# Performance work log

Hardware: AMD Instinct MI355X
Metric: run time of the kernel (lower is better)

## Reference

```python
import jax, jax.numpy as jnp
import numpy as np

# scipy.ndimage.gaussian_filter(sigma=1, truncate=4): radius 4, 9-tap kernel on EVERY axis
_R = 4
_xk = np.arange(-_R, _R + 1)
_wk = np.exp(-0.5 * _xk * _xk)
_W1D = (_wk / _wk.sum()).astype(np.float32)


def _sym_idx(n, r):
    # scipy 'reflect' (symmetric, edge repeated) extension indices for any r, any n
    p = np.arange(-r, n + r)
    q = np.mod(p, 2 * n)
    return np.where(q < n, q, 2 * n - 1 - q)


def gauss_filter(x):
    # separable sigma=1 Gaussian over ALL axes (incl. batch & channel), as scipy does
    w = jnp.asarray(_W1D)
    for axis in range(x.ndim):
        n = x.shape[axis]
        idx = jnp.asarray(_sym_idx(n, _R))
        xp = jnp.take(x, idx, axis=axis)  # symmetric-padded along `axis`
        acc = w[0] * jax.lax.slice_in_dim(xp, 0, n, axis=axis)
        for k in range(1, 2 * _R + 1):
            acc = acc + w[k] * jax.lax.slice_in_dim(xp, k, k + n, axis=axis)
        x = acc
    return x


def downsample(x):
    return x[:, :, ::2, ::2, ::2]


def upsample(x):
    # faithful to source: zero-interleave D and H, but zeros are APPENDED along W
    B, C, D, H, W = x.shape
    t = jnp.stack([x, jnp.zeros_like(x)], axis=3).reshape(B, C, 2 * D, H, W)
    t = jnp.stack([t, jnp.zeros_like(t)], axis=4).reshape(B, C, 2 * D, 2 * H, W)
    t = jnp.concatenate([t, jnp.zeros_like(t)], axis=4)  # (B,C,2D,2H,2W), 2nd W-half zero
    return gauss_filter(t * 8.0)


def lap_pyramid(img, max_levels):
    pyr = []
    cur = img
    for _ in range(max_levels):
        filt = gauss_filter(cur)
        down = downsample(filt)
        up = upsample(down)
        pyr.append(cur - up)
        cur = down
    return pyr


def setup_inputs():
    key = jax.random.key(0)
    k1, k2 = jax.random.split(key)
    shape = (2, 1, 64, 256, 256)
    return {
        "input": jax.random.normal(k1, shape, dtype=jnp.float32),
        "target": jax.random.normal(k2, shape, dtype=jnp.float32),
    }


def reference(input, target):
    max_levels = 5
    pyr_in = lap_pyramid(input, max_levels)
    pyr_tg = lap_pyramid(target, max_levels)
    loss = jnp.float32(0.0)
    for a, b in zip(pyr_in, pyr_tg):
        loss = loss + jnp.mean(jnp.abs(a - b))  # F.l1_loss (mean reduction)
    return loss
```

## Files before the change

kernel.cpp:

```cpp
#include <hip/hip_runtime.h>
#include <hip/hip_bf16.h>
#include <math.h>


struct GW { float w[9]; float A, B; };

__device__ __forceinline__ int ridx(int p, int n) {
    int m = 2 * n;
    int q = (p + m) & (m - 1);
    return (q < n) ? q : (m - 1 - q);
}

__device__ __forceinline__ float block_sum256(float v) {
    #pragma unroll
    for (int off = 32; off > 0; off >>= 1) v += __shfl_down(v, off, 64);
    __shared__ float wp[4];
    int tid = threadIdx.x;
    if ((tid & 63) == 0) wp[tid >> 6] = v;
    __syncthreads();
    return wp[0] + wp[1] + wp[2] + wp[3];
}

template<bool WDIFF>
__global__ __launch_bounds__(256)
void k1l0(const float* __restrict__ in, const float* __restrict__ tg,
          float* __restrict__ T1, __hip_bfloat16* __restrict__ DIFF, GW g)
{
    const int H = 256, W = 256, Wd = 128;
    const int x0d = blockIdx.x * 64, y0d = blockIdx.y * 16, slice = blockIdx.z;
    __shared__ float raw[40][136];
    __shared__ float mid[40][64];
    const size_t in_off  = (size_t)slice * H * W;
    const size_t out_off = (size_t)slice * 128 * 128;
    const int tid = threadIdx.x;
    const int gy0 = 2*y0d - 4, gx0 = 2*x0d - 4;
    for (int i = tid; i < 40*32; i += 256) {
        int rr = i >> 5, c4 = (i & 31) + 1;
        int gy = ridx(gy0 + rr, H);
        size_t base = in_off + (size_t)gy * W + gx0 + 4*c4;
        float4 v = *(const float4*)(in + base);
        float4 b = *(const float4*)(tg + base);
        v.x -= b.x; v.y -= b.y; v.z -= b.z; v.w -= b.w;
        *(float4*)&raw[rr][4*c4] = v;
    }
    for (int i = tid; i < 40*8; i += 256) {
        int rr = i >> 3, j = i & 7;
        int cc = (j < 4) ? j : (128 + j);
        int gy = ridx(gy0 + rr, H);
        int gx = ridx(gx0 + cc, W);
        size_t idx = in_off + (size_t)gy * W + gx;
        raw[rr][cc] = in[idx] - tg[idx];
    }
    __syncthreads();
    if (WDIFF) {
        for (int i = tid; i < 32*128; i += 256) {
            int r = i >> 7, c = i & 127;
            DIFF[in_off + (size_t)(2*y0d + r) * W + (2*x0d + c)] =
                __float2bfloat16(raw[4 + r][4 + c]);
        }
    }
    for (int i = tid; i < 40*64; i += 256) {
        int rr = i >> 6, c = i & 63;
        float s = 0.f;
        #pragma unroll
        for (int k = 0; k < 9; ++k) s = fmaf(g.w[k], raw[rr][2*c + k], s);
        mid[rr][c] = s;
    }
    __syncthreads();
    {
        int r = tid >> 6, c = tid & 63;
        int ox = x0d + c;
        #pragma unroll
        for (int j = 0; j < 4; ++j) {
            int oy = y0d + r*4 + j;
            int rb = 2*(r*4 + j);
            float s = 0.f;
            #pragma unroll
            for (int k = 0; k < 9; ++k) s = fmaf(g.w[k], mid[rb + k][c], s);
            T1[out_off + (size_t)oy * Wd + ox] = s;
        }
    }
}

__global__ __launch_bounds__(256)
void k2s(const float* __restrict__ Tin, float* __restrict__ Cout,
         int D, int Dd, int M4, GW g)
{
    long i = (long)blockIdx.x * 256 + threadIdx.x;
    if (i >= (long)Dd * M4) return;
    int zd = (int)(i / M4);
    int q  = (int)(i - (long)zd * M4);
    const float4* T = (const float4*)Tin;
    float4* O = (float4*)Cout;
    float4 s0 = {0,0,0,0}, s1 = {0,0,0,0};
    #pragma unroll
    for (int k = 0; k < 9; ++k) {
        int zp = 2*zd - 4 + k;
        int zk = (zp >= 0 && zp < D) ? zp : ridx(zp, D);
        float4 a = T[(size_t)zk * M4 + q];
        float4 b = T[(size_t)(D + zk) * M4 + q];
        s0.x = fmaf(g.w[k], a.x, s0.x); s0.y = fmaf(g.w[k], a.y, s0.y);
        s0.z = fmaf(g.w[k], a.z, s0.z); s0.w = fmaf(g.w[k], a.w, s0.w);
        s1.x = fmaf(g.w[k], b.x, s1.x); s1.y = fmaf(g.w[k], b.y, s1.y);
        s1.z = fmaf(g.w[k], b.z, s1.z); s1.w = fmaf(g.w[k], b.w, s1.w);
    }
    float4 o0, o1;
    o0.x = g.A*s0.x + g.B*s1.x; o0.y = g.A*s0.y + g.B*s1.y;
    o0.z = g.A*s0.z + g.B*s1.z; o0.w = g.A*s0.w + g.B*s1.w;
    o1.x = g.B*s0.x + g.A*s1.x; o1.y = g.B*s0.y + g.A*s1.y;
    o1.z = g.B*s0.z + g.A*s1.z; o1.w = g.B*s0.w + g.A*s1.w;
    O[(size_t)zd * M4 + q] = o0;
    O[(size_t)(Dd + zd) * M4 + q] = o1;
}

__global__ __launch_bounds__(256)
void k1s(const float* __restrict__ inA, float* __restrict__ out,
         int H, int W, int Hd, int Wd, GW g)
{
    const int x0d = blockIdx.x * 64, y0d = blockIdx.y * 16, slice = blockIdx.z;
    __shared__ float raw[40][136];
    __shared__ float mid[40][64];
    const size_t in_off  = (size_t)slice * H * W;
    const size_t out_off = (size_t)slice * Hd * Wd;
    const int tid = threadIdx.x;
    const int gy0 = 2*y0d - 4, gx0 = 2*x0d - 4;
    if (2*x0d + 127 < W) {
        for (int i = tid; i < 40*32; i += 256) {
            int rr = i >> 5, c4 = (i & 31) + 1;
            int gy = ridx(gy0 + rr, H);
            *(float4*)&raw[rr][4*c4] =
                *(const float4*)(inA + in_off + (size_t)gy * W + gx0 + 4*c4);
        }
        for (int i = tid; i < 40*8; i += 256) {
            int rr = i >> 3, j = i & 7;
            int cc = (j < 4) ? j : (128 + j);
            int gy = ridx(gy0 + rr, H), gx = ridx(gx0 + cc, W);
            raw[rr][cc] = inA[in_off + (size_t)gy * W + gx];
        }
    } else {
        for (int i = tid; i < 40*136; i += 256) {
            int rr = i / 136, cc = i - rr*136;
            int gy = ridx(gy0 + rr, H), gx = ridx(gx0 + cc, W);
            raw[rr][cc] = inA[in_off + (size_t)gy * W + gx];
        }
    }
    __syncthreads();
    for (int i = tid; i < 40*64; i += 256) {
        int rr = i >> 6, c = i & 63;
        float s = 0.f;
        #pragma unroll
        for (int k = 0; k < 9; ++k) s = fmaf(g.w[k], raw[rr][2*c + k], s);
        mid[rr][c] = s;
    }
    __syncthreads();
    {
        int r = tid >> 6, c = tid & 63;
        int ox = x0d + c;
        #pragma unroll
        for (int j = 0; j < 4; ++j) {
            int oy = y0d + r*4 + j;
            if (oy < Hd && ox < Wd) {
                int rb = 2*(r*4 + j);
                float s = 0.f;
                #pragma unroll
                for (int k = 0; k < 9; ++k) s = fmaf(g.w[k], mid[rb + k][c], s);
                out[out_off + (size_t)oy * Wd + ox] = s;
            }
        }
    }
}

struct K4P {
    const float* dn[5];
    const float* cur[5];
    const float* in; const float* tg;
    const __hip_bfloat16* DIFF;
    float* P;
    int use_diff;
    int bo[6];
    GW g;
};

__global__ __launch_bounds__(256)
void k4p(K4P p)
{
    const int Dt[5] = {64,32,16,8,4}, Ht[5] = {256,128,64,32,16};
    __shared__ float vt[20][72];
    __shared__ float mid[20][64];
    const int bid = (int)blockIdx.x;
    int l = 0;
    while (l < 4 && bid >= p.bo[l+1]) ++l;
    const int local = bid - p.bo[l];
    const int D = Dt[l], H = Ht[l], W = H;
    const int Dd = D >> 1, Hd = H >> 1, Wd = W >> 1, Md = Hd * Wd;
    const int ntx = (W + 63) >> 6, nty = (H + 31) >> 5;
    const int s = local / (ntx*nty);
    const int rem = local - s*(ntx*nty);
    const int ty = rem / ntx, tx = rem - ty*ntx;
    const int x0 = tx*64, y0 = ty*32;
    const int b = s / D, z = s - b*D;
    const GW g = p.g;
    const float* dn0 = p.dn[l] + (size_t)b * Dd * Md;
    const float* dn1 = p.dn[l] + (size_t)(1 - b) * Dd * Md;
    const int tid = threadIdx.x;
    const int vy0 = (y0 >> 1) - 2;

    const bool zin = (z >= 4) && (z + 4 < D);
    if (zin && !(z & 1)) {
        const int j0 = (z >> 1) - 2;
        for (int i = tid; i < 20*72; i += 256) {
            int rr = i / 72, cc = i - rr*72;
            int vy = vy0 + rr;
            int txx = x0 - 4 + cc;
            if (txx < 0) txx = -1 - txx;
            float v = 0.f;
            if (vy >= 0 && vy < Hd && txx < Wd) {
                size_t o = (size_t)vy * Wd + txx;
                float s0 = 0.f, s1 = 0.f;
                #pragma unroll
                for (int t = 0; t < 5; ++t) {
                    s0 = fmaf(g.w[2*t], dn0[(size_t)(j0 + t) * Md + o], s0);
                    s1 = fmaf(g.w[2*t], dn1[(size_t)(j0 + t) * Md + o], s1);
                }
                v = 8.f * (g.A*s0 + g.B*s1);
            }
            vt[rr][cc] = v;
        }
    } else if (zin) {
        const int j0 = (z - 3) >> 1;
        for (int i = tid; i < 20*72; i += 256) {
            int rr = i / 72, cc = i - rr*72;
            int vy = vy0 + rr;
            int txx = x0 - 4 + cc;
            if (txx < 0) txx = -1 - txx;
            float v = 0.f;
            if (vy >= 0 && vy < Hd && txx < Wd) {
                size_t o = (size_t)vy * Wd + txx;
                float s0 = 0.f, s1 = 0.f;
                #pragma unroll
                for (int t = 0; t < 4; ++t) {
                    s0 = fmaf(g.w[2*t+1], dn0[(size_t)(j0 + t) * Md + o], s0);
                    s1 = fmaf(g.w[2*t+1], dn1[(size_t)(j0 + t) * Md + o], s1);
                }
                v = 8.f * (g.A*s0 + g.B*s1);
            }
            vt[rr][cc] = v;
        }
    } else {
        for (int i = tid; i < 20*72; i += 256) {
            int rr = i / 72, cc = i - rr*72;
            int vy = vy0 + rr;
            int txx = x0 - 4 + cc;
            if (txx < 0) txx = -1 - txx;
            float v = 0.f;
            if (vy >= 0 && vy < Hd && txx < Wd) {
                size_t o = (size_t)vy * Wd + txx;
                float s0 = 0.f, s1 = 0.f;
                #pragma unroll
                for (int k = 0; k < 9; ++k) {
                    int zk = ridx(z - 4 + k, D);
                    if (!(zk & 1)) {
                        int j = zk >> 1;
                        s0 = fmaf(g.w[k], dn0[(size_t)j * Md + o], s0);
                        s1 = fmaf(g.w[k], dn1[(size_t)j * Md + o], s1);
                    }
                }
                v = 8.f * (g.A*s0 + g.B*s1);
            }
            vt[rr][cc] = v;
        }
    }
    __syncthreads();
    for (int i = tid; i < 20*64; i += 256) {
        int rr = i >> 6, c = i & 63;
        float sv = 0.f;
        #pragma unroll
        for (int k = 0; k < 9; ++k) sv = fmaf(g.w[k], vt[rr][c + k], sv);
        mid[rr][c] = sv;
    }
    __syncthreads();
    const bool yin = (y0 >= 4) && (y0 + 35 < H);
    const int c = tid & 63;
    const int ry_base = (tid >> 6) * 8;
    const int ox = x0 + c;
    const size_t c_off = (size_t)s * H * W;
    const float* curl = (l >= 1) ? p.cur[l] : nullptr;
    float lsum = 0.f;
    #pragma unroll
    for (int j = 0; j < 8; ++j) {
        int ry = ry_base + j;
        int oy = y0 + ry;
        if (ox < W && oy < H) {
            float sv = 0.f;
            if (yin) {
                if (!(j & 1)) {
                    int r0 = ry >> 1;
                    sv = g.w[0]*mid[r0][c] + g.w[2]*mid[r0+1][c] + g.w[4]*mid[r0+2][c]
                       + g.w[6]*mid[r0+3][c] + g.w[8]*mid[r0+4][c];
                } else {
                    int r0 = ((ry - 3) >> 1) + 2;
                    sv = g.w[1]*mid[r0][c] + g.w[3]*mid[r0+1][c]
                       + g.w[5]*mid[r0+2][c] + g.w[7]*mid[r0+3][c];
                }
            } else {
                #pragma unroll
                for (int k = 0; k < 9; ++k) {
                    int gy = ridx(oy - 4 + k, H);
                    if (!(gy & 1)) sv = fmaf(g.w[k], mid[(gy >> 1) - vy0][c], sv);
                }
            }
            size_t idx = c_off + (size_t)oy * W + ox;
            float cv;
            if (l == 0) cv = p.use_diff ? __bfloat162float(p.DIFF[idx])
                                        : (p.in[idx] - p.tg[idx]);
            else        cv = curl[idx];
            lsum += fabsf(cv - sv);
        }
    }
    float tot = block_sum256(lsum);
    if (tid == 0) p.P[bid] = tot / ((float)(2*D) * H * W);
}

__global__ __launch_bounds__(1024)
void kreduce(const float* __restrict__ P, int n, float* __restrict__ out)
{
    float s = 0.f;
    for (int i = threadIdx.x; i < n; i += 1024) s += P[i];
    #pragma unroll
    for (int off = 32; off > 0; off >>= 1) s += __shfl_down(s, off, 64);
    __shared__ float wp[16];
    if ((threadIdx.x & 63) == 0) wp[threadIdx.x >> 6] = s;
    __syncthreads();
    if (threadIdx.x == 0) {
        float t = 0.f;
        #pragma unroll
        for (int w = 0; w < 16; ++w) t += wp[w];
        out[0] = t;
    }
}

extern "C" void kernel_launch(void* const* d_in, const int* in_sizes, int n_in,
                              void* d_out, int out_size, void* d_ws, size_t ws_size,
                              hipStream_t stream)
{
    const float* in = (const float*)d_in[0];
    const float* tg = (const float*)d_in[1];
    float* out = (float*)d_out;

    GW g;
    {
        double u[9], S = 0.0;
        for (int k = 0; k < 9; ++k) { double d = k - 4; u[k] = exp(-0.5 * d * d); S += u[k]; }
        for (int k = 0; k < 9; ++k) g.w[k] = (float)(u[k] / S);
        g.A = (float)((2.0*u[0] + u[1] + u[3] + u[4]) / S);
        g.B = (float)((u[1] + 2.0*u[2] + u[3]) / S);
    }

    float* T1  = (float*)d_ws;
    float* C1  = T1  + 2097152;
    float* C2  = C1  + 1048576;
    float* C3  = C2  + 131072;
    float* C4  = C3  + 16384;
    float* C5  = C4  + 2048;
    float* Tl1 = C5  + 256;
    float* Tl2 = Tl1 + 262144;
    float* Tl3 = Tl2 + 32768;
    float* Tl4 = Tl3 + 4096;
    float* P   = Tl4 + 512;
    float* wend = P + 8192;
    __hip_bfloat16* DIFF = (__hip_bfloat16*)wend;
    const size_t base_bytes = (size_t)((char*)wend - (char*)d_ws);
    const size_t diff_bytes = (size_t)2 * 64 * 256 * 256 * sizeof(__hip_bfloat16);
    const int use_diff = (ws_size >= base_bytes + diff_bytes) ? 1 : 0;

    dim3 blk(256);

    if (use_diff) k1l0<true ><<<dim3(2,8,128), blk, 0, stream>>>(in, tg, T1, DIFF, g);
    else          k1l0<false><<<dim3(2,8,128), blk, 0, stream>>>(in, tg, T1, nullptr, g);

    k2s<<<dim3(512), blk, 0, stream>>>(T1, C1, 64, 32, 4096, g);

    k1s<<<dim3(1,4,64), blk, 0, stream>>>(C1, Tl1, 128, 128, 64, 64, g);
    k2s<<<dim3(64),     blk, 0, stream>>>(Tl1, C2, 32, 16, 1024, g);
    k1s<<<dim3(1,2,32), blk, 0, stream>>>(C2, Tl2, 64, 64, 32, 32, g);
    k2s<<<dim3(8),      blk, 0, stream>>>(Tl2, C3, 16, 8, 256, g);
    k1s<<<dim3(1,1,16), blk, 0, stream>>>(C3, Tl3, 32, 32, 16, 16, g);
    k2s<<<dim3(1),      blk, 0, stream>>>(Tl3, C4, 8, 4, 64, g);
    k1s<<<dim3(1,1,8),  blk, 0, stream>>>(C4, Tl4, 16, 16, 8, 8, g);
    k2s<<<dim3(1),      blk, 0, stream>>>(Tl4, C5, 4, 2, 16, g);

    K4P prm;
    prm.dn[0] = C1; prm.dn[1] = C2; prm.dn[2] = C3; prm.dn[3] = C4; prm.dn[4] = C5;
    prm.cur[0] = nullptr; prm.cur[1] = C1; prm.cur[2] = C2; prm.cur[3] = C3; prm.cur[4] = C4;
    prm.in = in; prm.tg = tg;
    prm.DIFF = use_diff ? DIFF : nullptr;
    prm.P = P; prm.use_diff = use_diff;
    prm.g = g;
    prm.bo[0] = 0; prm.bo[1] = 4096; prm.bo[2] = 4608;
    prm.bo[3] = 4672; prm.bo[4] = 4688; prm.bo[5] = 4696;
    k4p<<<dim3(4696), blk, 0, stream>>>(prm);

    kreduce<<<1, 1024, 0, stream>>>(P, 4696, out);
}
```

Baseline: 119.2 us.

## Pair z-slices per block, share depth loads, and exploit zero W-half in level 0

The level-0 loss blocks now cover only the x range affected by the upsampled signal, which is nonzero in just the first W-half plus the filter halo. For the rest of that half, where the upsample is zero, k1l0 sums |in-tg| directly into the partials. The bf16 DIFF write is shrunk to match. k4pz handles two adjacent z slices per block, so the even and odd depth taps come from one set of float4 loads of the downsampled volume, and the vt/mid tiles are doubled. This cuts grid size and global reads, at the cost of more shared memory and register pressure per block.

```diff
diff --git a/kernel.cpp b/kernel.cpp
--- a/kernel.cpp
+++ b/kernel.cpp
@@ -24,7 +24,8 @@
 template<bool WDIFF>
 __global__ __launch_bounds__(256)
 void k1l0(const float* __restrict__ in, const float* __restrict__ tg,
-          float* __restrict__ T1, __hip_bfloat16* __restrict__ DIFF, GW g)
+          float* __restrict__ T1, __hip_bfloat16* __restrict__ DIFF,
+          float* __restrict__ P, GW g)
 {
     const int H = 256, W = 256, Wd = 128;
     const int x0d = blockIdx.x * 64, y0d = blockIdx.y * 16, slice = blockIdx.z;
@@ -53,11 +54,29 @@
     }
     __syncthreads();
     if (WDIFF) {
-        for (int i = tid; i < 32*128; i += 256) {
-            int r = i >> 7, c = i & 127;
-            DIFF[in_off + (size_t)(2*y0d + r) * W + (2*x0d + c)] =
-                __float2bfloat16(raw[4 + r][4 + c]);
-        }
+        if (blockIdx.x == 0) {
+            for (int i = tid; i < 32*128; i += 256) {
+                int r = i >> 7, c = i & 127;
+                DIFF[in_off + (size_t)(2*y0d + r) * W + c] =
+                    __float2bfloat16(raw[4 + r][4 + c]);
+            }
+        } else {
+            for (int i = tid; i < 32*4; i += 256) {
+                int r = i >> 2, c = i & 3;
+                DIFF[in_off + (size_t)(2*y0d + r) * W + 128 + c] =
+                    __float2bfloat16(raw[4 + r][4 + c]);
+            }
+        }
+    }
+    if (blockIdx.x == 1) {
+        float lsum = 0.f;
+        for (int i = tid; i < 32*124; i += 256) {
+            int r = i / 124, c = i - r*124;
+            lsum += fabsf(raw[4 + r][8 + c]);
+        }
+        float tot = block_sum256(lsum);
+        if (tid == 0)
+            P[blockIdx.y + 8*blockIdx.z] = tot * (1.f / 8388608.f);
     }
     for (int i = tid; i < 40*64; i += 256) {
         int rr = i >> 6, c = i & 63;
@@ -182,143 +201,200 @@
 };
 
 __global__ __launch_bounds__(256)
-void k4p(K4P p)
+void k4pz(K4P p)
 {
     const int Dt[5] = {64,32,16,8,4}, Ht[5] = {256,128,64,32,16};
-    __shared__ float vt[20][72];
-    __shared__ float mid[20][64];
+    __shared__ float vt[2][20][72];
+    __shared__ float mid[2][20][64];
     const int bid = (int)blockIdx.x;
     int l = 0;
     while (l < 4 && bid >= p.bo[l+1]) ++l;
     const int local = bid - p.bo[l];
     const int D = Dt[l], H = Ht[l], W = H;
     const int Dd = D >> 1, Hd = H >> 1, Wd = W >> 1, Md = Hd * Wd;
-    const int ntx = (W + 63) >> 6, nty = (H + 31) >> 5;
-    const int s = local / (ntx*nty);
-    const int rem = local - s*(ntx*nty);
-    const int ty = rem / ntx, tx = rem - ty*ntx;
-    const int x0 = tx*64, y0 = ty*32;
-    const int b = s / D, z = s - b*D;
+    const int ntx = (l == 0) ? 3 : ((W + 63) >> 6);
+    const int nty = (H + 31) >> 5;
+    const int ntiles = ntx * nty;
+    const int pairidx = local / ntiles;
+    const int rem = local - pairidx * ntiles;
+    const int ty = rem / ntx, tx = rem - ty * ntx;
+    const int x0 = tx * 64, y0 = ty * 32;
+    const int b = pairidx / Dd, m = pairidx - b * Dd;
+    const int z0 = 2 * m;
     const GW g = p.g;
     const float* dn0 = p.dn[l] + (size_t)b * Dd * Md;
     const float* dn1 = p.dn[l] + (size_t)(1 - b) * Dd * Md;
     const int tid = threadIdx.x;
     const int vy0 = (y0 >> 1) - 2;
 
-    const bool zin = (z >= 4) && (z + 4 < D);
-    if (zin && !(z & 1)) {
-        const int j0 = (z >> 1) - 2;
-        for (int i = tid; i < 20*72; i += 256) {
-            int rr = i / 72, cc = i - rr*72;
+    const bool fastz = (z0 >= 4) && (z0 + 5 < D);
+    if (fastz) {
+        const int j0 = m - 2;
+        for (int i = tid; i < 20*18; i += 256) {
+            int rr = i / 18, gg = i - rr*18;
             int vy = vy0 + rr;
-            int txx = x0 - 4 + cc;
-            if (txx < 0) txx = -1 - txx;
-            float v = 0.f;
-            if (vy >= 0 && vy < Hd && txx < Wd) {
-                size_t o = (size_t)vy * Wd + txx;
-                float s0 = 0.f, s1 = 0.f;
+            bool vyok = (vy >= 0) && (vy < Hd);
+            if (gg == 0) {
                 #pragma unroll
-                for (int t = 0; t < 5; ++t) {
-                    s0 = fmaf(g.w[2*t], dn0[(size_t)(j0 + t) * Md + o], s0);
-                    s1 = fmaf(g.w[2*t], dn1[(size_t)(j0 + t) * Md + o], s1);
+                for (int cc = 0; cc < 4; ++cc) {
+                    int txx = x0 - 4 + cc;
+                    if (txx < 0) txx = -1 - txx;
+                    float e0=0.f, e1=0.f, o0=0.f, o1=0.f;
+                    if (vyok && txx < Wd) {
+                        size_t o = (size_t)vy * Wd + txx;
+                        #pragma unroll
+                        for (int t = 0; t < 5; ++t) {
+                            float a  = dn0[(size_t)(j0+t)*Md + o];
+                            float bb = dn1[(size_t)(j0+t)*Md + o];
+                            float we = g.w[2*t];
+                            e0 = fmaf(we, a, e0); e1 = fmaf(we, bb, e1);
+                            if (t >= 1) {
+                                float wo = g.w[2*t-1];
+                                o0 = fmaf(wo, a, o0); o1 = fmaf(wo, bb, o1);
+                            }
+                        }
+                    }
+                    vt[0][rr][cc] = 8.f*(g.A*e0 + g.B*e1);
+                    vt[1][rr][cc] = 8.f*(g.A*o0 + g.B*o1);
                 }
-                v = 8.f * (g.A*s0 + g.B*s1);
-            }
-            vt[rr][cc] = v;
-        }
-    } else if (zin) {
-        const int j0 = (z - 3) >> 1;
-        for (int i = tid; i < 20*72; i += 256) {
-            int rr = i / 72, cc = i - rr*72;
-            int vy = vy0 + rr;
-            int txx = x0 - 4 + cc;
-            if (txx < 0) txx = -1 - txx;
-            float v = 0.f;
-            if (vy >= 0 && vy < Hd && txx < Wd) {
-                size_t o = (size_t)vy * Wd + txx;
-                float s0 = 0.f, s1 = 0.f;
-                #pragma unroll
-                for (int t = 0; t < 4; ++t) {
-                    s0 = fmaf(g.w[2*t+1], dn0[(size_t)(j0 + t) * Md + o], s0);
-                    s1 = fmaf(g.w[2*t+1], dn1[(size_t)(j0 + t) * Md + o], s1);
+            } else {
+                int cc = 4 * gg;
+                int txx = x0 - 4 + cc;
+                if (vyok && txx + 3 < Wd) {
+                    size_t o = (size_t)vy * Wd + txx;
+                    float4 e0={0,0,0,0}, e1={0,0,0,0}, o0={0,0,0,0}, o1={0,0,0,0};
+                    #pragma unroll
+                    for (int t = 0; t < 5; ++t) {
+                        float4 a  = *(const float4*)(dn0 + (size_t)(j0+t)*Md + o);
+                        float4 bb = *(const float4*)(dn1 + (size_t)(j0+t)*Md + o);
+                        float we = g.w[2*t];
+                        e0.x=fmaf(we,a.x,e0.x); e0.y=fmaf(we,a.y,e0.y);
+                        e0.z=fmaf(we,a.z,e0.z); e0.w=fmaf(we,a.w,e0.w);
+                        e1.x=fmaf(we,bb.x,e1.x); e1.y=fmaf(we,bb.y,e1.y);
+                        e1.z=fmaf(we,bb.z,e1.z); e1.w=fmaf(we,bb.w,e1.w);
+                        if (t >= 1) {
+                            float wo = g.w[2*t-1];
+                            o0.x=fmaf(wo,a.x,o0.x); o0.y=fmaf(wo,a.y,o0.y);
+                            o0.z=fmaf(wo,a.z,o0.z); o0.w=fmaf(wo,a.w,o0.w);
+                            o1.x=fmaf(wo,bb.x,o1.x); o1.y=fmaf(wo,bb.y,o1.y);
+                            o1.z=fmaf(wo,bb.z,o1.z); o1.w=fmaf(wo,bb.w,o1.w);
+                        }
+                    }
+                    vt[0][rr][cc+0] = 8.f*(g.A*e0.x + g.B*e1.x);
+                    vt[0][rr][cc+1] = 8.f*(g.A*e0.y + g.B*e1.y);
+                    vt[0][rr][cc+2] = 8.f*(g.A*e0.z + g.B*e1.z);
+                    vt[0][rr][cc+3] = 8.f*(g.A*e0.w + g.B*e1.w);
+                    vt[1][rr][cc+0] = 8.f*(g.A*o0.x + g.B*o1.x);
+                    vt[1][rr][cc+1] = 8.f*(g.A*o0.y + g.B*o1.y);
+                    vt[1][rr][cc+2] = 8.f*(g.A*o0.z + g.B*o1.z);
+                    vt[1][rr][cc+3] = 8.f*(g.A*o0.w + g.B*o1.w);
+                } else {
+                    #pragma unroll
+                    for (int q4 = 0; q4 < 4; ++q4) {
+                        int txq = txx + q4;
+                        float e0=0.f, e1=0.f, o0=0.f, o1=0.f;
+                        if (vyok && txq < Wd) {
+                            size_t o = (size_t)vy * Wd + txq;
+                            #pragma unroll
+                            for (int t = 0; t < 5; ++t) {
+                                float a  = dn0[(size_t)(j0+t)*Md + o];
+                                float bb = dn1[(size_t)(j0+t)*Md + o];
+                                float we = g.w[2*t];
+                                e0 = fmaf(we, a, e0); e1 = fmaf(we, bb, e1);
+                                if (t >= 1) {
+                                    float wo = g.w[2*t-1];
+                                    o0 = fmaf(wo, a, o0); o1 = fmaf(wo, bb, o1);
+                                }
+                            }
+                        }
+                        vt[0][rr][cc+q4] = 8.f*(g.A*e0 + g.B*e1);
+                        vt[1][rr][cc+q4] = 8.f*(g.A*o0 + g.B*o1);
+                    }
                 }
-                v = 8.f * (g.A*s0 + g.B*s1);
-            }
-            vt[rr][cc] = v;
+            }
         }
     } else {
-        for (int i = tid; i < 20*72; i += 256) {
-            int rr = i / 72, cc = i - rr*72;
-            int vy = vy0 + rr;
-            int txx = x0 - 4 + cc;
-            if (txx < 0) txx = -1 - txx;
-            float v = 0.f;
-            if (vy >= 0 && vy < Hd && txx < Wd) {
-                size_t o = (size_t)vy * Wd + txx;
-                float s0 = 0.f, s1 = 0.f;
-                #pragma unroll
-                for (int k = 0; k < 9; ++k) {
-                    int zk = ridx(z - 4 + k, D);
-                    if (!(zk & 1)) {
-                        int j = zk >> 1;
-                        s0 = fmaf(g.w[k], dn0[(size_t)j * Md + o], s0);
-                        s1 = fmaf(g.w[k], dn1[(size_t)j * Md + o], s1);
-                    }
+        for (int zz = 0; zz < 2; ++zz) {
+            int z = z0 + zz;
+            for (int i = tid; i < 20*72; i += 256) {
+                int rr = i / 72, cc = i - rr*72;
+                int vy = vy0 + rr;
+                int txx = x0 - 4 + cc;
+                if (txx < 0) txx = -1 - txx;
+                float v = 0.f;
+                if (vy >= 0 && vy < Hd && txx < Wd) {
+                    size_t o = (size_t)vy * Wd + txx;
+                    float s0 = 0.f, s1 = 0.f;
+                    #pragma unroll
+                    for (int k = 0; k < 9; ++k) {
+                        int zk = ridx(z - 4 + k, D);
+                        if (!(zk & 1)) {
+                            int j = zk >> 1;
+                            s0 = fmaf(g.w[k], dn0[(size_t)j * Md + o], s0);
+                            s1 = fmaf(g.w[k], dn1[(size_t)j * Md + o], s1);
+                        }
+                    }
+                    v = 8.f * (g.A*s0 + g.B*s1);
                 }
-                v = 8.f * (g.A*s0 + g.B*s1);
-            }
-            vt[rr][cc] = v;
-        }
-    }
-    __syncthreads();
-    for (int i = tid; i < 20*64; i += 256) {
-        int rr = i >> 6, c = i & 63;
+                vt[zz][rr][cc] = v;
+            }
+        }
+    }
+    __syncthreads();
+    for (int i = tid; i < 2*20*64; i += 256) {
+        int zz = i / 1280;
+        int r2 = i - zz*1280;
+        int rr = r2 >> 6, c = r2 & 63;
         float sv = 0.f;
         #pragma unroll
-        for (int k = 0; k < 9; ++k) sv = fmaf(g.w[k], vt[rr][c + k], sv);
-        mid[rr][c] = sv;
+        for (int k = 0; k < 9; ++k) sv = fmaf(g.w[k], vt[zz][rr][c + k], sv);
+        mid[zz][rr][c] = sv;
     }
     __syncthreads();
     const bool yin = (y0 >= 4) && (y0 + 35 < H);
     const int c = tid & 63;
     const int ry_base = (tid >> 6) * 8;
     const int ox = x0 + c;
-    const size_t c_off = (size_t)s * H * W;
+    const int xlim = (l == 0) ? 132 : W;
     const float* curl = (l >= 1) ? p.cur[l] : nullptr;
     float lsum = 0.f;
-    #pragma unroll
-    for (int j = 0; j < 8; ++j) {
-        int ry = ry_base + j;
-        int oy = y0 + ry;
-        if (ox < W && oy < H) {
-            float sv = 0.f;
-            if (yin) {
-                if (!(j & 1)) {
-                    int r0 = ry >> 1;
-                    sv = g.w[0]*mid[r0][c] + g.w[2]*mid[r0+1][c] + g.w[4]*mid[r0+2][c]
-                       + g.w[6]*mid[r0+3][c] + g.w[8]*mid[r0+4][c];
+    for (int zz = 0; zz < 2; ++zz) {
+        const size_t c_off = (size_t)(b*D + z0 + zz) * H * W;
+        #pragma unroll
+        for (int j = 0; j < 8; ++j) {
+            int ry = ry_base + j;
+            int oy = y0 + ry;
+            if (ox < xlim && oy < H) {
+                float sv = 0.f;
+                if (yin) {
+                    if (!(j & 1)) {
+                        int r0 = ry >> 1;
+                        sv = g.w[0]*mid[zz][r0][c] + g.w[2]*mid[zz][r0+1][c]
+                           + g.w[4]*mid[zz][r0+2][c] + g.w[6]*mid[zz][r0+3][c]
+                           + g.w[8]*mid[zz][r0+4][c];
+                    } else {
+                        int r0 = ((ry - 3) >> 1) + 2;
+                        sv = g.w[1]*mid[zz][r0][c] + g.w[3]*mid[zz][r0+1][c]
+                           + g.w[5]*mid[zz][r0+2][c] + g.w[7]*mid[zz][r0+3][c];
+                    }
                 } else {
-                    int r0 = ((ry - 3) >> 1) + 2;
-                    sv = g.w[1]*mid[r0][c] + g.w[3]*mid[r0+1][c]
-                       + g.w[5]*mid[r0+2][c] + g.w[7]*mid[r0+3][c];
+                    #pragma unroll
+                    for (int k = 0; k < 9; ++k) {
+                        int gy = ridx(oy - 4 + k, H);
+                        if (!(gy & 1)) sv = fmaf(g.w[k], mid[zz][(gy >> 1) - vy0][c], sv);
+                    }
                 }
-            } else {
-                #pragma unroll
-                for (int k = 0; k < 9; ++k) {
-                    int gy = ridx(oy - 4 + k, H);
-                    if (!(gy & 1)) sv = fmaf(g.w[k], mid[(gy >> 1) - vy0][c], sv);
-                }
-            }
-            size_t idx = c_off + (size_t)oy * W + ox;
-            float cv;
-            if (l == 0) cv = p.use_diff ? __bfloat162float(p.DIFF[idx])
-                                        : (p.in[idx] - p.tg[idx]);
-            else        cv = curl[idx];
-            lsum += fabsf(cv - sv);
+                size_t idx = c_off + (size_t)oy * W + ox;
+                float cv;
+                if (l == 0) cv = p.use_diff ? __bfloat162float(p.DIFF[idx])
+                                            : (p.in[idx] - p.tg[idx]);
+                else        cv = curl[idx];
+                lsum += fabsf(cv - sv);
+            }
         }
     }
     float tot = block_sum256(lsum);
-    if (tid == 0) p.P[bid] = tot / ((float)(2*D) * H * W);
+    if (tid == 0) p.P[1024 + bid] = tot / ((float)(2*D) * H * W);
 }
 
 __global__ __launch_bounds__(1024)
@@ -367,7 +443,7 @@
     float* Tl3 = Tl2 + 32768;
     float* Tl4 = Tl3 + 4096;
     float* P   = Tl4 + 512;
-    float* wend = P + 8192;
+    float* wend = P + 4096;
     __hip_bfloat16* DIFF = (__hip_bfloat16*)wend;
     const size_t base_bytes = (size_t)((char*)wend - (char*)d_ws);
     const size_t diff_bytes = (size_t)2 * 64 * 256 * 256 * sizeof(__hip_bfloat16);
@@ -375,8 +451,8 @@
 
     dim3 blk(256);
 
-    if (use_diff) k1l0<true ><<<dim3(2,8,128), blk, 0, stream>>>(in, tg, T1, DIFF, g);
-    else          k1l0<false><<<dim3(2,8,128), blk, 0, stream>>>(in, tg, T1, nullptr, g);
+    if (use_diff) k1l0<true ><<<dim3(2,8,128), blk, 0, stream>>>(in, tg, T1, DIFF, P, g);
+    else          k1l0<false><<<dim3(2,8,128), blk, 0, stream>>>(in, tg, T1, nullptr, P, g);
 
     k2s<<<dim3(512), blk, 0, stream>>>(T1, C1, 64, 32, 4096, g);
 
@@ -396,9 +472,9 @@
     prm.DIFF = use_diff ? DIFF : nullptr;
     prm.P = P; prm.use_diff = use_diff;
     prm.g = g;
-    prm.bo[0] = 0; prm.bo[1] = 4096; prm.bo[2] = 4608;
-    prm.bo[3] = 4672; prm.bo[4] = 4688; prm.bo[5] = 4696;
-    k4p<<<dim3(4696), blk, 0, stream>>>(prm);
-
-    kreduce<<<1, 1024, 0, stream>>>(P, 4696, out);
-}
+    prm.bo[0] = 0; prm.bo[1] = 1536; prm.bo[2] = 1792;
+    prm.bo[3] = 1824; prm.bo[4] = 1832; prm.bo[5] = 1836;
+    k4pz<<<dim3(1836), blk, 0, stream>>>(prm);
+
+    kreduce<<<1, 1024, 0, stream>>>(P, 1024 + 1836, out);
+}
```

Result: slower. 122.7 us (+2.9%).

## Exploit zero right-half of upsample to skip level-0 work and precompute depth-upsampled volumes

Applied to the files above, without the earlier changes.

The upsampled level-0 image has a zero right W-half, so beyond column 132 the residual equals the raw difference. That region's L1 sum is now computed directly in the first kernel, and the pyramid loss kernel covers only three x-tiles at level 0. The depth-axis upsample filter for levels 0-2 is precomputed into new V buffers by a fused kernel that runs alongside the next level's downsample. This removes redundant per-tile depth filtering, at the cost of extra workspace and extra global writes and reads for V.

```diff
diff --git a/kernel.cpp b/kernel.cpp
--- a/kernel.cpp
+++ b/kernel.cpp
@@ -24,7 +24,8 @@
 template<bool WDIFF>
 __global__ __launch_bounds__(256)
 void k1l0(const float* __restrict__ in, const float* __restrict__ tg,
-          float* __restrict__ T1, __hip_bfloat16* __restrict__ DIFF, GW g)
+          float* __restrict__ T1, __hip_bfloat16* __restrict__ DIFF,
+          float* __restrict__ P, GW g)
 {
     const int H = 256, W = 256, Wd = 128;
     const int x0d = blockIdx.x * 64, y0d = blockIdx.y * 16, slice = blockIdx.z;
@@ -53,11 +54,29 @@
     }
     __syncthreads();
     if (WDIFF) {
-        for (int i = tid; i < 32*128; i += 256) {
-            int r = i >> 7, c = i & 127;
-            DIFF[in_off + (size_t)(2*y0d + r) * W + (2*x0d + c)] =
-                __float2bfloat16(raw[4 + r][4 + c]);
-        }
+        if (blockIdx.x == 0) {
+            for (int i = tid; i < 32*128; i += 256) {
+                int r = i >> 7, c = i & 127;
+                DIFF[in_off + (size_t)(2*y0d + r) * W + c] =
+                    __float2bfloat16(raw[4 + r][4 + c]);
+            }
+        } else {
+            for (int i = tid; i < 32*4; i += 256) {
+                int r = i >> 2, c = i & 3;
+                DIFF[in_off + (size_t)(2*y0d + r) * W + 128 + c] =
+                    __float2bfloat16(raw[4 + r][4 + c]);
+            }
+        }
+    }
+    if (blockIdx.x == 1) {
+        float lsum = 0.f;
+        for (int i = tid; i < 32*124; i += 256) {
+            int r = i / 124, c = i - r*124;
+            lsum += fabsf(raw[4 + r][8 + c]);
+        }
+        float tot = block_sum256(lsum);
+        if (tid == 0)
+            P[blockIdx.y + 8*blockIdx.z] = tot * (1.f / 8388608.f);
     }
     for (int i = tid; i < 40*64; i += 256) {
         int rr = i >> 6, c = i & 63;
@@ -113,11 +132,10 @@
     O[(size_t)(Dd + zd) * M4 + q] = o1;
 }
 
-__global__ __launch_bounds__(256)
-void k1s(const float* __restrict__ inA, float* __restrict__ out,
-         int H, int W, int Hd, int Wd, GW g)
-{
-    const int x0d = blockIdx.x * 64, y0d = blockIdx.y * 16, slice = blockIdx.z;
+__device__ void dev_k1_slice(const float* __restrict__ inA, float* __restrict__ out,
+                             int x0d, int y0d, int slice, int H, int W, int Hd, int Wd,
+                             const GW& g)
+{
     __shared__ float raw[40][136];
     __shared__ float mid[40][64];
     const size_t in_off  = (size_t)slice * H * W;
@@ -170,8 +188,78 @@
     }
 }
 
+__global__ __launch_bounds__(256)
+void k1s(const float* __restrict__ inA, float* __restrict__ out,
+         int H, int W, int Hd, int Wd, GW g)
+{
+    dev_k1_slice(inA, out, blockIdx.x*64, blockIdx.y*16, blockIdx.z, H, W, Hd, Wd, g);
+}
+
+__device__ void dev_k3_elem(long i, const float4* __restrict__ Dn, float4* __restrict__ O,
+                            int D, int Dd, int M4, const GW& g)
+{
+    if (i >= (long)D * M4) return;
+    int z = (int)(i / M4);
+    int q = (int)(i - (long)z * M4);
+    float4 s0 = {0,0,0,0}, s1 = {0,0,0,0};
+    auto f4 = [](float4& a, float w, const float4 b) {
+        a.x = fmaf(w, b.x, a.x); a.y = fmaf(w, b.y, a.y);
+        a.z = fmaf(w, b.z, a.z); a.w = fmaf(w, b.w, a.w);
+    };
+    if (z >= 4 && z + 4 < D) {
+        if ((z & 1) == 0) {
+            int base = (z >> 1) - 2;
+            #pragma unroll
+            for (int kk = 0; kk < 5; ++kk) {
+                f4(s0, g.w[2*kk], Dn[(size_t)(base + kk) * M4 + q]);
+                f4(s1, g.w[2*kk], Dn[(size_t)(Dd + base + kk) * M4 + q]);
+            }
+        } else {
+            int base = (z - 3) >> 1;
+            #pragma unroll
+            for (int kk = 0; kk < 4; ++kk) {
+                f4(s0, g.w[2*kk+1], Dn[(size_t)(base + kk) * M4 + q]);
+                f4(s1, g.w[2*kk+1], Dn[(size_t)(Dd + base + kk) * M4 + q]);
+            }
+        }
+    } else {
+        #pragma unroll
+        for (int k = 0; k < 9; ++k) {
+            int zk = ridx(z - 4 + k, D);
+            if (!(zk & 1)) {
+                int j = zk >> 1;
+                f4(s0, g.w[k], Dn[(size_t)j * M4 + q]);
+                f4(s1, g.w[k], Dn[(size_t)(Dd + j) * M4 + q]);
+            }
+        }
+    }
+    float4 o0, o1;
+    o0.x = 8.f*(g.A*s0.x + g.B*s1.x); o0.y = 8.f*(g.A*s0.y + g.B*s1.y);
+    o0.z = 8.f*(g.A*s0.z + g.B*s1.z); o0.w = 8.f*(g.A*s0.w + g.B*s1.w);
+    o1.x = 8.f*(g.B*s0.x + g.A*s1.x); o1.y = 8.f*(g.B*s0.y + g.A*s1.y);
+    o1.z = 8.f*(g.B*s0.z + g.A*s1.z); o1.w = 8.f*(g.B*s0.w + g.A*s1.w);
+    O[(size_t)z * M4 + q] = o0;
+    O[(size_t)(D + z) * M4 + q] = o1;
+}
+
+__global__ __launch_bounds__(256)
+void fatk(const float* __restrict__ k1in, float* __restrict__ k1out,
+          int H, int W, int Hd, int Wd, int nty, int n1,
+          const float* __restrict__ dn, float* __restrict__ V,
+          int D, int Dd, int M4, GW g)
+{
+    if ((int)blockIdx.x < n1) {
+        int ty = (int)blockIdx.x % nty, slice = (int)blockIdx.x / nty;
+        dev_k1_slice(k1in, k1out, 0, ty*16, slice, H, W, Hd, Wd, g);
+    } else {
+        long i = (long)((int)blockIdx.x - n1)*256 + threadIdx.x;
+        dev_k3_elem(i, (const float4*)dn, (float4*)V, D, Dd, M4, g);
+    }
+}
+
 struct K4P {
-    const float* dn[5];
+    const float* V[3];
+    const float* dn34[2];
     const float* cur[5];
     const float* in; const float* tg;
     const __hip_bfloat16* DIFF;
@@ -182,7 +270,7 @@
 };
 
 __global__ __launch_bounds__(256)
-void k4p(K4P p)
+void k4all(K4P p)
 {
     const int Dt[5] = {64,32,16,8,4}, Ht[5] = {256,128,64,32,16};
     __shared__ float vt[20][72];
@@ -193,60 +281,33 @@
     const int local = bid - p.bo[l];
     const int D = Dt[l], H = Ht[l], W = H;
     const int Dd = D >> 1, Hd = H >> 1, Wd = W >> 1, Md = Hd * Wd;
-    const int ntx = (W + 63) >> 6, nty = (H + 31) >> 5;
+    const int ntx = (l == 0) ? 3 : ((W + 63) >> 6);
+    const int nty = (H + 31) >> 5;
     const int s = local / (ntx*nty);
     const int rem = local - s*(ntx*nty);
     const int ty = rem / ntx, tx = rem - ty*ntx;
     const int x0 = tx*64, y0 = ty*32;
     const int b = s / D, z = s - b*D;
     const GW g = p.g;
-    const float* dn0 = p.dn[l] + (size_t)b * Dd * Md;
-    const float* dn1 = p.dn[l] + (size_t)(1 - b) * Dd * Md;
     const int tid = threadIdx.x;
     const int vy0 = (y0 >> 1) - 2;
 
-    const bool zin = (z >= 4) && (z + 4 < D);
-    if (zin && !(z & 1)) {
-        const int j0 = (z >> 1) - 2;
+    if (l < 3) {
+        const float* V = p.V[l];
+        const size_t v_off = (size_t)s * Md;
         for (int i = tid; i < 20*72; i += 256) {
             int rr = i / 72, cc = i - rr*72;
             int vy = vy0 + rr;
             int txx = x0 - 4 + cc;
             if (txx < 0) txx = -1 - txx;
             float v = 0.f;
-            if (vy >= 0 && vy < Hd && txx < Wd) {
-                size_t o = (size_t)vy * Wd + txx;
-                float s0 = 0.f, s1 = 0.f;
-                #pragma unroll
-                for (int t = 0; t < 5; ++t) {
-                    s0 = fmaf(g.w[2*t], dn0[(size_t)(j0 + t) * Md + o], s0);
-                    s1 = fmaf(g.w[2*t], dn1[(size_t)(j0 + t) * Md + o], s1);
-                }
-                v = 8.f * (g.A*s0 + g.B*s1);
-            }
+            if (vy >= 0 && vy < Hd && txx < Wd) v = V[v_off + (size_t)vy * Wd + txx];
             vt[rr][cc] = v;
         }
-    } else if (zin) {
-        const int j0 = (z - 3) >> 1;
-        for (int i = tid; i < 20*72; i += 256) {
-            int rr = i / 72, cc = i - rr*72;
-            int vy = vy0 + rr;
-            int txx = x0 - 4 + cc;
-            if (txx < 0) txx = -1 - txx;
-            float v = 0.f;
-            if (vy >= 0 && vy < Hd && txx < Wd) {
-                size_t o = (size_t)vy * Wd + txx;
-                float s0 = 0.f, s1 = 0.f;
-                #pragma unroll
-                for (int t = 0; t < 4; ++t) {
-                    s0 = fmaf(g.w[2*t+1], dn0[(size_t)(j0 + t) * Md + o], s0);
-                    s1 = fmaf(g.w[2*t+1], dn1[(size_t)(j0 + t) * Md + o], s1);
-                }
-                v = 8.f * (g.A*s0 + g.B*s1);
-            }
-            vt[rr][cc] = v;
-        }
     } else {
+        const float* dnb = p.dn34[l-3];
+        const float* dn0 = dnb + (size_t)b * Dd * Md;
+        const float* dn1 = dnb + (size_t)(1 - b) * Dd * Md;
         for (int i = tid; i < 20*72; i += 256) {
             int rr = i / 72, cc = i - rr*72;
             int vy = vy0 + rr;
@@ -283,6 +344,7 @@
     const int c = tid & 63;
     const int ry_base = (tid >> 6) * 8;
     const int ox = x0 + c;
+    const int xlim = (l == 0) ? 132 : W;
     const size_t c_off = (size_t)s * H * W;
     const float* curl = (l >= 1) ? p.cur[l] : nullptr;
     float lsum = 0.f;
@@ -290,7 +352,7 @@
     for (int j = 0; j < 8; ++j) {
         int ry = ry_base + j;
         int oy = y0 + ry;
-        if (ox < W && oy < H) {
+        if (ox < xlim && oy < H) {
             float sv = 0.f;
             if (yin) {
                 if (!(j & 1)) {
@@ -318,7 +380,7 @@
         }
     }
     float tot = block_sum256(lsum);
-    if (tid == 0) p.P[bid] = tot / ((float)(2*D) * H * W);
+    if (tid == 0) p.P[1024 + bid] = tot / ((float)(2*D) * H * W);
 }
 
 __global__ __launch_bounds__(1024)
@@ -366,7 +428,10 @@
     float* Tl2 = Tl1 + 262144;
     float* Tl3 = Tl2 + 32768;
     float* Tl4 = Tl3 + 4096;
-    float* P   = Tl4 + 512;
+    float* V0  = Tl4 + 512;
+    float* V1  = V0  + 2097152;
+    float* V2  = V1  + 262144;
+    float* P   = V2  + 32768;
     float* wend = P + 8192;
     __hip_bfloat16* DIFF = (__hip_bfloat16*)wend;
     const size_t base_bytes = (size_t)((char*)wend - (char*)d_ws);
@@ -375,30 +440,37 @@
 
     dim3 blk(256);
 
-    if (use_diff) k1l0<true ><<<dim3(2,8,128), blk, 0, stream>>>(in, tg, T1, DIFF, g);
-    else          k1l0<false><<<dim3(2,8,128), blk, 0, stream>>>(in, tg, T1, nullptr, g);
+    if (use_diff) k1l0<true ><<<dim3(2,8,128), blk, 0, stream>>>(in, tg, T1, DIFF, P, g);
+    else          k1l0<false><<<dim3(2,8,128), blk, 0, stream>>>(in, tg, T1, nullptr, P, g);
 
     k2s<<<dim3(512), blk, 0, stream>>>(T1, C1, 64, 32, 4096, g);
 
-    k1s<<<dim3(1,4,64), blk, 0, stream>>>(C1, Tl1, 128, 128, 64, 64, g);
-    k2s<<<dim3(64),     blk, 0, stream>>>(Tl1, C2, 32, 16, 1024, g);
-    k1s<<<dim3(1,2,32), blk, 0, stream>>>(C2, Tl2, 64, 64, 32, 32, g);
-    k2s<<<dim3(8),      blk, 0, stream>>>(Tl2, C3, 16, 8, 256, g);
-    k1s<<<dim3(1,1,16), blk, 0, stream>>>(C3, Tl3, 32, 32, 16, 16, g);
-    k2s<<<dim3(1),      blk, 0, stream>>>(Tl3, C4, 8, 4, 64, g);
-    k1s<<<dim3(1,1,8),  blk, 0, stream>>>(C4, Tl4, 16, 16, 8, 8, g);
-    k2s<<<dim3(1),      blk, 0, stream>>>(Tl4, C5, 4, 2, 16, g);
+    fatk<<<dim3(256 + 1024), blk, 0, stream>>>(C1, Tl1, 128, 128, 64, 64, 4, 256,
+                                               C1, V0, 64, 32, 4096, g);
+    k2s<<<dim3(64), blk, 0, stream>>>(Tl1, C2, 32, 16, 1024, g);
+
+    fatk<<<dim3(64 + 128), blk, 0, stream>>>(C2, Tl2, 64, 64, 32, 32, 2, 64,
+                                             C2, V1, 32, 16, 1024, g);
+    k2s<<<dim3(8), blk, 0, stream>>>(Tl2, C3, 16, 8, 256, g);
+
+    fatk<<<dim3(16 + 16), blk, 0, stream>>>(C3, Tl3, 32, 32, 16, 16, 1, 16,
+                                            C3, V2, 16, 8, 256, g);
+    k2s<<<dim3(1), blk, 0, stream>>>(Tl3, C4, 8, 4, 64, g);
+
+    k1s<<<dim3(1,1,8), blk, 0, stream>>>(C4, Tl4, 16, 16, 8, 8, g);
+    k2s<<<dim3(1), blk, 0, stream>>>(Tl4, C5, 4, 2, 16, g);
 
     K4P prm;
-    prm.dn[0] = C1; prm.dn[1] = C2; prm.dn[2] = C3; prm.dn[3] = C4; prm.dn[4] = C5;
+    prm.V[0] = V0; prm.V[1] = V1; prm.V[2] = V2;
+    prm.dn34[0] = C4; prm.dn34[1] = C5;
     prm.cur[0] = nullptr; prm.cur[1] = C1; prm.cur[2] = C2; prm.cur[3] = C3; prm.cur[4] = C4;
     prm.in = in; prm.tg = tg;
     prm.DIFF = use_diff ? DIFF : nullptr;
     prm.P = P; prm.use_diff = use_diff;
     prm.g = g;
-    prm.bo[0] = 0; prm.bo[1] = 4096; prm.bo[2] = 4608;
-    prm.bo[3] = 4672; prm.bo[4] = 4688; prm.bo[5] = 4696;
-    k4p<<<dim3(4696), blk, 0, stream>>>(prm);
-
-    kreduce<<<1, 1024, 0, stream>>>(P, 4696, out);
-}
+    prm.bo[0] = 0; prm.bo[1] = 3072; prm.bo[2] = 3584;
+    prm.bo[3] = 3648; prm.bo[4] = 3664; prm.bo[5] = 3672;
+    k4all<<<dim3(3672), blk, 0, stream>>>(prm);
+
+    kreduce<<<1, 1024, 0, stream>>>(P, 1024 + 3672, out);
+}
```

Result: faster. 102.2 us (-14.3%).
